# Performance work log

Hardware: AMD Instinct MI355X
Metric: run time of the kernel (lower is better)

Reference implementation:

```python
import jax, jax.numpy as jnp
import numpy as np

BN_EPS = 1e-5
SAMPLE_KEY = jax.random.key(42)


def setup_inputs() -> dict:
    key = jax.random.key(0)
    ks = jax.random.split(key, 12)
    B, W, E = 524288, 8, 4
    D = W * E  # 32, input dim of fc1

    def lin(k, fan_in, fan_out):
        k1, k2 = jax.random.split(k)
        bound = 1.0 / np.sqrt(fan_in)
        w = jax.random.uniform(k1, (fan_in, fan_out), jnp.float32, -bound, bound)
        b = jax.random.uniform(k2, (fan_out,), jnp.float32, -bound, bound)
        return w, b

    W1, b1 = lin(ks[0], D, 50)
    W2, b2 = lin(ks[1], 50, 30)
    W3, b3 = lin(ks[2], 30, 20)
    W4, b4 = lin(ks[3], 20, 15)
    W5, b5 = lin(ks[4], 15, W)
    # BatchNorm affine params (eval mode, running_mean=0, running_var=1)
    g1, be1 = jnp.ones((50,), jnp.float32), jnp.zeros((50,), jnp.float32)
    g2, be2 = jnp.ones((30,), jnp.float32), jnp.zeros((30,), jnp.float32)
    g3, be3 = jnp.ones((20,), jnp.float32), jnp.zeros((20,), jnp.float32)
    events = jax.random.normal(ks[5], (B, W, E), jnp.float32)
    return {"events": events,
            "W1": W1, "b1": b1, "g1": g1, "be1": be1,
            "W2": W2, "b2": b2, "g2": g2, "be2": be2,
            "W3": W3, "b3": b3, "g3": g3, "be3": be3,
            "W4": W4, "b4": b4, "W5": W5, "b5": b5}


def _bn_eval(x, g, b):
    # eval-mode BatchNorm1d with running_mean=0, running_var=1
    return x * (g / jnp.sqrt(1.0 + BN_EPS)) + b


def _probs(events, W1, b1, g1, be1, W2, b2, g2, be2, W3, b3, g3, be3, W4, b4, W5, b5):
    B = events.shape[0]
    x = events.reshape(B, -1)  # (B, window*event_size)
    h = jax.nn.relu(_bn_eval(x @ W1 + b1, g1, be1))
    h = jax.nn.relu(_bn_eval(h @ W2 + b2, g2, be2))
    h = jax.nn.relu(_bn_eval(h @ W3 + b3, g3, be3))
    h = jax.nn.relu(h @ W4 + b4)
    return jax.nn.sigmoid(h @ W5 + b5)  # (B, window_size)


def reference(events, W1, b1, g1, be1, W2, b2, g2, be2, W3, b3, g3, be3, W4, b4, W5, b5):
    p = _probs(events, W1, b1, g1, be1, W2, b2, g2, be2, W3, b3, g3, be3, W4, b4, W5, b5)
    # np.random.choice([0,1], p=[p, 1-p]) => P(choice=1) = 1 - p
    choice = jax.random.bernoulli(SAMPLE_KEY, 1.0 - p).astype(p.dtype)  # (B, W)
    chosen_events_np = 1.0 - choice
    flipped = jnp.abs(choice - p)            # prob of sampled outcome per element
    log_prob = jnp.log(jnp.prod(flipped, axis=1))  # (B,)
    return chosen_events_np, log_prob
```

## Files before the change

### kernel.cpp

```cpp
#include <hip/hip_runtime.h>
#include <math.h>

#define THREADS 256
#define TPW 4
#define ROWS_PER_BLOCK 256
#define P_MARGIN 2e-4f
#define FIXCAP 64

typedef float f32x4 __attribute__((ext_vector_type(4)));
typedef short short8 __attribute__((ext_vector_type(8)));
union Frag { unsigned u[4]; short8 s; };

#define FR1 0
#define FR2 2048
#define FR3 4096
#define FR4 5120
#define FR5 6144
#define VB1 6656
#define VS1 6708
#define VE1 6760
#define VB2 6812
#define VS2 6844
#define VE2 6876
#define VB3 6908
#define VS3 6928
#define VE3 6948
#define VB4 6968
#define VB5 6984
#define PZ  6992
#define WPOOL 7024

__device__ __forceinline__ void tf2x32(unsigned x0, unsigned x1,
                                       unsigned &o0, unsigned &o1) {
  const unsigned k0 = 0u;
  const unsigned k1 = 42u;
  const unsigned k2 = 0x1BD11BDAu ^ k0 ^ k1;
  x0 += k0; x1 += k1;
#define TF_R(r) { x0 += x1; x1 = (x1 << (r)) | (x1 >> (32 - (r))); x1 ^= x0; }
  TF_R(13) TF_R(15) TF_R(26) TF_R(6)
  x0 += k1; x1 += k2 + 1u;
  TF_R(17) TF_R(29) TF_R(16) TF_R(24)
  x0 += k2; x1 += k0 + 2u;
  TF_R(13) TF_R(15) TF_R(26) TF_R(6)
  x0 += k0; x1 += k1 + 3u;
  TF_R(17) TF_R(29) TF_R(16) TF_R(24)
  x0 += k1; x1 += k2 + 4u;
  TF_R(13) TF_R(15) TF_R(26) TF_R(6)
  x0 += k2; x1 += k0 + 5u;
#undef TF_R
  o0 = x0; o1 = x1;
}

__device__ __forceinline__ unsigned rtnb(float v) {
  unsigned b = __float_as_uint(v);
  return (b + 0x7FFFu + ((b >> 16) & 1u)) & 0xFFFF0000u;
}

__device__ __forceinline__ unsigned cvtpk(float a, float b) {
  unsigned r;
  asm("v_cvt_pk_bf16_f32 %0, %1, %2" : "=v"(r) : "v"(a), "v"(b));
  return r;
}

__device__ __forceinline__ void pack8(const float f[8], short8 &H, short8 &L) {
  Frag h, l;
#pragma unroll
  for (int d = 0; d < 4; ++d) {
    unsigned hd = cvtpk(f[2 * d], f[2 * d + 1]);
    h.u[d] = hd;
    float r0 = f[2 * d]     - __uint_as_float(hd << 16);
    float r1 = f[2 * d + 1] - __uint_as_float(hd & 0xFFFF0000u);
    l.u[d] = cvtpk(r0, r1);
  }
  H = h.s; L = l.s;
}

__device__ __forceinline__ f32x4 mfma16(short8 a, short8 b, f32x4 c) {
  return __builtin_amdgcn_mfma_f32_16x16x32_bf16(a, b, c, 0, 0, 0);
}

__device__ __forceinline__ short8 ldfrag(const float *sW, int dwoff) {
  return *reinterpret_cast<const short8 *>(sW + dwoff);
}
__device__ __forceinline__ f32x4 ldv4(const float *sW, int dwoff) {
  return *reinterpret_cast<const f32x4 *>(sW + dwoff);
}

template <int K, int N, int NT, int FB, bool PERM>
__device__ __forceinline__ void stageA(const float *__restrict__ W,
                                       float *sW, int t) {
  for (int i = t; i < K * N; i += THREADS) {
    int k = i / N, n = i - k * N;
    float v = W[i];
    unsigned hb = rtnb(v);
    unsigned lb = rtnb(v - __uint_as_float(hb));
    int kt = k >> 5, g = (k >> 3) & 3, e = k & 7, d = e >> 1, par = e & 1;
    int tile, r;
    if (PERM) {
      int pg = n >> 5, m = n & 31, tt = (m >> 2) & 1;
      r = ((m >> 3) << 2) | (m & 3);
      tile = pg * 2 + tt;
    } else {
      tile = n >> 4; r = n & 15;
    }
    int lane = g * 16 + r;
    int dwhi = FB + (kt * NT + tile) * 512 + lane * 4 + d;
    unsigned short *hp = reinterpret_cast<unsigned short *>(sW);
    hp[2 * dwhi + par] = (unsigned short)(hb >> 16);
    hp[2 * (dwhi + 256) + par] = (unsigned short)(lb >> 16);
  }
}

__device__ __forceinline__ void bnpack(f32x4 a0, f32x4 a1, const float *sW,
                                       int vs, int ve, int g,
                                       short8 &H, short8 &L) {
  f32x4 sc0 = ldv4(sW, vs + g * 8),     of0 = ldv4(sW, ve + g * 8);
  f32x4 sc1 = ldv4(sW, vs + g * 8 + 4), of1 = ldv4(sW, ve + g * 8 + 4);
  float f[8];
#pragma unroll
  for (int q = 0; q < 4; ++q) {
    f[q]     = fmaxf(fmaf(a0[q], sc0[q], of0[q]), 0.f);
    f[4 + q] = fmaxf(fmaf(a1[q], sc1[q], of1[q]), 0.f);
  }
  pack8(f, H, L);
}

__global__ __launch_bounds__(THREADS, 2)
void wtf_kernel(const float* __restrict__ events,
                const float* __restrict__ W1, const float* __restrict__ b1,
                const float* __restrict__ g1, const float* __restrict__ be1,
                const float* __restrict__ W2, const float* __restrict__ b2,
                const float* __restrict__ g2, const float* __restrict__ be2,
                const float* __restrict__ W3, const float* __restrict__ b3,
                const float* __restrict__ g3, const float* __restrict__ be3,
                const float* __restrict__ W4, const float* __restrict__ b4,
                const float* __restrict__ W5, const float* __restrict__ b5,
                float* __restrict__ out_chosen,
                float* __restrict__ out_logp,
                int B) {
  __shared__ float sW[WPOOL];
  __shared__ unsigned s_cnt;
  __shared__ unsigned s_rows[FIXCAP];
  __shared__ double sA[64];
  __shared__ double sB[64];
  __shared__ double sF[8];

  const int t = threadIdx.x;
  const float rden = (float)(1.0 / sqrt(1.0 + 1e-5));

  if (t == 0) s_cnt = 0;
  for (int i = t; i < WPOOL; i += THREADS) sW[i] = 0.f;
  __syncthreads();
  stageA<32, 50, 4, FR1, true>(W1, sW, t);
  stageA<50, 30, 2, FR2, true>(W2, sW, t);
  stageA<30, 20, 2, FR3, true>(W3, sW, t);
  stageA<20, 15, 2, FR4, true>(W4, sW, t);
  stageA<15,  8, 1, FR5, false>(W5, sW, t);
  if (t < 50)                  { sW[VB1 + t] = b1[t]; sW[VS1 + t] = g1[t] * rden; sW[VE1 + t] = be1[t]; }
  else if (t >= 64 && t < 94)  { int i = t - 64;  sW[VB2 + i] = b2[i]; sW[VS2 + i] = g2[i] * rden; sW[VE2 + i] = be2[i]; }
  else if (t >= 128 && t < 148){ int i = t - 128; sW[VB3 + i] = b3[i]; sW[VS3 + i] = g3[i] * rden; sW[VE3 + i] = be3[i]; }
  else if (t >= 192 && t < 207){ sW[VB4 + (t - 192)] = b4[t - 192]; }
  else if (t >= 224 && t < 232){ sW[VB5 + (t - 224)] = b5[t - 224]; }
  __syncthreads();

  const int w = t >> 6, lane = t & 63;
  const int c = lane & 15, g = lane >> 4;
  const int labase = lane * 4;

  const int wrow0 = blockIdx.x * ROWS_PER_BLOCK + w * (TPW * 16);
  const float4 *xp = reinterpret_cast<const float4 *>(
      events + (size_t)(wrow0 + c) * 32 + g * 8);

  f32x4 aa[TPW];

#pragma unroll
  for (int tt = 0; tt < TPW; ++tt) {
    float4 xa = xp[tt * 128], xb = xp[tt * 128 + 1];
    float xf[8] = {xa.x, xa.y, xa.z, xa.w, xb.x, xb.y, xb.z, xb.w};
    short8 Xh, Xl; pack8(xf, Xh, Xl);

    f32x4 a1[4];
#pragma unroll
    for (int ti = 0; ti < 4; ++ti) {
      f32x4 acc = ldv4(sW, VB1 + (ti >> 1) * 32 + g * 8 + (ti & 1) * 4);
      short8 wh = ldfrag(sW, FR1 + ti * 512 + labase);
      short8 wl = ldfrag(sW, FR1 + ti * 512 + 256 + labase);
      acc = mfma16(wh, Xl, acc);
      acc = mfma16(wl, Xh, acc);
      a1[ti] = mfma16(wh, Xh, acc);
    }

    short8 B2h[2], B2l[2];
    bnpack(a1[0], a1[1], sW, VS1,      VE1,      g, B2h[0], B2l[0]);
    bnpack(a1[2], a1[3], sW, VS1 + 32, VE1 + 32, g, B2h[1], B2l[1]);

    f32x4 a2[2];
#pragma unroll
    for (int ti = 0; ti < 2; ++ti) {
      f32x4 acc = ldv4(sW, VB2 + g * 8 + ti * 4);
#pragma unroll
      for (int kt = 0; kt < 2; ++kt) {
        short8 wh = ldfrag(sW, FR2 + (kt * 2 + ti) * 512 + labase);
        short8 wl = ldfrag(sW, FR2 + (kt * 2 + ti) * 512 + 256 + labase);
        acc = mfma16(wh, B2l[kt], acc);
        acc = mfma16(wl, B2h[kt], acc);
        acc = mfma16(wh, B2h[kt], acc);
      }
      a2[ti] = acc;
    }

    short8 B3h, B3l;
    bnpack(a2[0], a2[1], sW, VS2, VE2, g, B3h, B3l);

    f32x4 a3[2];
#pragma unroll
    for (int ti = 0; ti < 2; ++ti) {
      f32x4 acc = ldv4(sW, VB3 + g * 8 + ti * 4);
      short8 wh = ldfrag(sW, FR3 + ti * 512 + labase);
      short8 wl = ldfrag(sW, FR3 + ti * 512 + 256 + labase);
      acc = mfma16(wh, B3l, acc);
      acc = mfma16(wl, B3h, acc);
      a3[ti] = mfma16(wh, B3h, acc);
    }

    short8 B4h, B4l;
    bnpack(a3[0], a3[1], sW, VS3, VE3, g, B4h, B4l);

    f32x4 a4[2];
#pragma unroll
    for (int ti = 0; ti < 2; ++ti) {
      f32x4 acc = ldv4(sW, VB4 + g * 8 + ti * 4);
      short8 wh = ldfrag(sW, FR4 + ti * 512 + labase);
      short8 wl = ldfrag(sW, FR4 + ti * 512 + 256 + labase);
      acc = mfma16(wh, B4l, acc);
      acc = mfma16(wl, B4h, acc);
      a4[ti] = mfma16(wh, B4h, acc);
    }

    short8 B5h, B5l;
    {
      float f[8];
#pragma unroll
      for (int q = 0; q < 4; ++q) {
        f[q]     = fmaxf(a4[0][q], 0.f);
        f[4 + q] = fmaxf(a4[1][q], 0.f);
      }
      pack8(f, B5h, B5l);
    }

    {
      f32x4 acc = ldv4(sW, VB5 + g * 4);
      short8 wh = ldfrag(sW, FR5 + labase);
      short8 wl = ldfrag(sW, FR5 + 256 + labase);
      acc = mfma16(wh, B5l, acc);
      acc = mfma16(wl, B5h, acc);
      aa[tt] = mfma16(wh, B5h, acc);
    }
  }

#pragma unroll
  for (int tt = 0; tt < TPW; ++tt) {
    const int row = wrow0 + tt * 16 + c;
    float s2v = __shfl_xor(aa[tt][2], 32);
    float s3v = __shfl_xor(aa[tt][3], 32);
    float l0 = (g < 2) ? aa[tt][0] : s2v;
    float l1 = (g < 2) ? aa[tt][1] : s3v;
    const int base = ((g & 1) << 2) | ((g >> 1) << 1);
    float p0 = 1.f / (1.f + __expf(-l0));
    float p1 = 1.f / (1.f + __expf(-l1));
    unsigned o0, o1, q0, q1;
    tf2x32(0u, 8u * (unsigned)row + (unsigned)base,      o0, o1);
    tf2x32(0u, 8u * (unsigned)row + (unsigned)base + 1u, q0, q1);
    float u0 = __uint_as_float(0x3F800000u | ((o0 ^ o1) >> 9)) - 1.f;
    float u1 = __uint_as_float(0x3F800000u | ((q0 ^ q1) >> 9)) - 1.f;
    float th0 = 1.f - p0, th1 = 1.f - p1;
    bool c0 = u0 < th0, c1 = u1 < th1;
    bool need = (fabsf(u0 - th0) < P_MARGIN) || (fabsf(u1 - th1) < P_MARGIN);
    float prod = (c0 ? th0 : p0) * (c1 ? th1 : p1);
    prod *= __shfl_xor(prod, 16);
    prod *= __shfl_xor(prod, 32);
    float2 chv = make_float2(c0 ? 0.f : 1.f, c1 ? 0.f : 1.f);
    *reinterpret_cast<float2 *>(out_chosen + (size_t)row * 8 + base) = chv;
    if (g == 0) out_logp[row] = __logf(prod);
    if (need) {
      unsigned i = atomicAdd(&s_cnt, 1u);
      if (i < FIXCAP) s_rows[i] = (unsigned)row;
    }
  }

  __syncthreads();
  unsigned cnt = s_cnt;
  if (cnt > FIXCAP) cnt = FIXCAP;
  if (cnt == 0) return;

  const double denom = sqrt(1.0 + 1e-5);
  for (unsigned r = 0; r < cnt; ++r) {
    const int rb = (int)s_rows[r];

    if (t < 32) sA[t] = (double)events[(size_t)rb * 32 + t];
    __syncthreads();

    double v = 0.0;
    if (t < 50) {
#pragma unroll
      for (int k = 0; k < 32; ++k) v = fma(sA[k], (double)W1[k * 50 + t], v);
      v += (double)b1[t];
      v = v * ((double)g1[t] / denom) + (double)be1[t];
      v = v > 0.0 ? v : 0.0;
    }
    __syncthreads();
    if (t < 50) sB[t] = v;
    __syncthreads();

    v = 0.0;
    if (t < 30) {
#pragma unroll
      for (int k = 0; k < 50; ++k) v = fma(sB[k], (double)W2[k * 30 + t], v);
      v += (double)b2[t];
      v = v * ((double)g2[t] / denom) + (double)be2[t];
      v = v > 0.0 ? v : 0.0;
    }
    __syncthreads();
    if (t < 30) sA[t] = v;
    __syncthreads();

    v = 0.0;
    if (t < 20) {
#pragma unroll
      for (int k = 0; k < 30; ++k) v = fma(sA[k], (double)W3[k * 20 + t], v);
      v += (double)b3[t];
      v = v * ((double)g3[t] / denom) + (double)be3[t];
      v = v > 0.0 ? v : 0.0;
    }
    __syncthreads();
    if (t < 20) sB[t] = v;
    __syncthreads();

    v = 0.0;
    if (t < 15) {
#pragma unroll
      for (int k = 0; k < 20; ++k) v = fma(sB[k], (double)W4[k * 15 + t], v);
      v += (double)b4[t];
      v = v > 0.0 ? v : 0.0;
    }
    __syncthreads();
    if (t < 15) sA[t] = v;
    __syncthreads();

    if (t < 8) {
      v = 0.0;
#pragma unroll
      for (int k = 0; k < 15; ++k) v = fma(sA[k], (double)W5[k * 8 + t], v);
      v += (double)b5[t];
      double p = 1.0 / (1.0 + exp(-v));
      unsigned j = 8u * (unsigned)rb + (unsigned)t, o0, o1;
      tf2x32(0u, j, o0, o1);
      unsigned bits = o0 ^ o1;
      float u = __uint_as_float(0x3F800000u | (bits >> 9)) - 1.f;
      double thr = 1.0 - p;
      bool choice = ((double)u < thr);
      out_chosen[(size_t)rb * 8 + t] = choice ? 0.f : 1.f;
      sF[t] = choice ? thr : p;
    }
    __syncthreads();
    if (t == 0) {
      double prod = 1.0;
      for (int w2 = 0; w2 < 8; ++w2) prod *= sF[w2];
      out_logp[rb] = (float)log(prod);
    }
    __syncthreads();
  }
}

extern "C" void kernel_launch(void* const* d_in, const int* in_sizes, int n_in,
                              void* d_out, int out_size, void* d_ws, size_t ws_size,
                              hipStream_t stream) {
  const float* events = (const float*)d_in[0];
  const float* W1  = (const float*)d_in[1];
  const float* b1  = (const float*)d_in[2];
  const float* g1  = (const float*)d_in[3];
  const float* be1 = (const float*)d_in[4];
  const float* W2  = (const float*)d_in[5];
  const float* b2  = (const float*)d_in[6];
  const float* g2  = (const float*)d_in[7];
  const float* be2 = (const float*)d_in[8];
  const float* W3  = (const float*)d_in[9];
  const float* b3  = (const float*)d_in[10];
  const float* g3  = (const float*)d_in[11];
  const float* be3 = (const float*)d_in[12];
  const float* W4  = (const float*)d_in[13];
  const float* b4  = (const float*)d_in[14];
  const float* W5  = (const float*)d_in[15];
  const float* b5  = (const float*)d_in[16];

  const int B = in_sizes[0] / 32;
  float* out = (float*)d_out;
  float* out_chosen = out;
  float* out_logp   = out + (size_t)B * 8;

  const int blocks = (B + ROWS_PER_BLOCK - 1) / ROWS_PER_BLOCK;
  hipLaunchKernelGGL(wtf_kernel, dim3(blocks), dim3(THREADS), 0, stream,
                     events, W1, b1, g1, be1, W2, b2, g2, be2,
                     W3, b3, g3, be3, W4, b4, W5, b5,
                     out_chosen, out_logp, B);
}
```

Before: 216.1 us.

## Prebuild packed weight image once and hoist layer-4/5 fragments to registers

Adds a single-block pack kernel that converts all weights into the split-bf16 MFMA fragment layout in a workspace buffer. Each main-kernel block then copies that image into LDS with float4 loads, replacing the per-block zeroing, scatter and conversion. The small layer-4 and layer-5 weight fragments are also loaded once into registers instead of being reread from LDS on every tile. The cost is an extra kernel launch, a dependency on the workspace being large enough (with a fallback when it is not), and added register pressure.

```diff
diff --git a/kernel.cpp b/kernel.cpp
--- a/kernel.cpp
+++ b/kernel.cpp
@@ -86,9 +86,9 @@
   return *reinterpret_cast<const f32x4 *>(sW + dwoff);
 }
 
-template <int K, int N, int NT, int FB, bool PERM>
+template <int K, int N, int NT, int FB>
 __device__ __forceinline__ void stageA(const float *__restrict__ W,
-                                       float *sW, int t) {
+                                       unsigned short *hp, int t, bool perm) {
   for (int i = t; i < K * N; i += THREADS) {
     int k = i / N, n = i - k * N;
     float v = W[i];
@@ -96,7 +96,7 @@
     unsigned lb = rtnb(v - __uint_as_float(hb));
     int kt = k >> 5, g = (k >> 3) & 3, e = k & 7, d = e >> 1, par = e & 1;
     int tile, r;
-    if (PERM) {
+    if (perm) {
       int pg = n >> 5, m = n & 31, tt = (m >> 2) & 1;
       r = ((m >> 3) << 2) | (m & 3);
       tile = pg * 2 + tt;
@@ -105,24 +105,45 @@
     }
     int lane = g * 16 + r;
     int dwhi = FB + (kt * NT + tile) * 512 + lane * 4 + d;
-    unsigned short *hp = reinterpret_cast<unsigned short *>(sW);
     hp[2 * dwhi + par] = (unsigned short)(hb >> 16);
     hp[2 * (dwhi + 256) + par] = (unsigned short)(lb >> 16);
   }
 }
 
-__device__ __forceinline__ void bnpack(f32x4 a0, f32x4 a1, const float *sW,
-                                       int vs, int ve, int g,
-                                       short8 &H, short8 &L) {
-  f32x4 sc0 = ldv4(sW, vs + g * 8),     of0 = ldv4(sW, ve + g * 8);
-  f32x4 sc1 = ldv4(sW, vs + g * 8 + 4), of1 = ldv4(sW, ve + g * 8 + 4);
-  float f[8];
-#pragma unroll
-  for (int q = 0; q < 4; ++q) {
-    f[q]     = fmaxf(fmaf(a0[q], sc0[q], of0[q]), 0.f);
-    f[4 + q] = fmaxf(fmaf(a1[q], sc1[q], of1[q]), 0.f);
-  }
-  pack8(f, H, L);
+__device__ __forceinline__ void build_image(
+    float *img, int t,
+    const float *W1, const float *b1, const float *g1, const float *be1,
+    const float *W2, const float *b2, const float *g2, const float *be2,
+    const float *W3, const float *b3, const float *g3, const float *be3,
+    const float *W4, const float *b4, const float *W5, const float *b5) {
+  const float rden = (float)(1.0 / sqrt(1.0 + 1e-5));
+  for (int i = t; i < WPOOL; i += THREADS) img[i] = 0.f;
+  __syncthreads();
+  unsigned short *hp = reinterpret_cast<unsigned short *>(img);
+  stageA<32, 50, 4, FR1>(W1, hp, t, true);
+  stageA<50, 30, 2, FR2>(W2, hp, t, true);
+  stageA<30, 20, 2, FR3>(W3, hp, t, true);
+  stageA<20, 15, 2, FR4>(W4, hp, t, true);
+  stageA<15,  8, 1, FR5>(W5, hp, t, false);
+  if (t < 50)                  { img[VB1 + t] = b1[t]; img[VS1 + t] = g1[t] * rden; img[VE1 + t] = be1[t]; }
+  else if (t >= 64 && t < 94)  { int i = t - 64;  img[VB2 + i] = b2[i]; img[VS2 + i] = g2[i] * rden; img[VE2 + i] = be2[i]; }
+  else if (t >= 128 && t < 148){ int i = t - 128; img[VB3 + i] = b3[i]; img[VS3 + i] = g3[i] * rden; img[VE3 + i] = be3[i]; }
+  else if (t >= 192 && t < 207){ img[VB4 + (t - 192)] = b4[t - 192]; }
+  else if (t >= 224 && t < 232){ img[VB5 + (t - 224)] = b5[t - 224]; }
+}
+
+__global__ __launch_bounds__(THREADS, 1)
+void pack_kernel(const float* __restrict__ W1, const float* __restrict__ b1,
+                 const float* __restrict__ g1, const float* __restrict__ be1,
+                 const float* __restrict__ W2, const float* __restrict__ b2,
+                 const float* __restrict__ g2, const float* __restrict__ be2,
+                 const float* __restrict__ W3, const float* __restrict__ b3,
+                 const float* __restrict__ g3, const float* __restrict__ be3,
+                 const float* __restrict__ W4, const float* __restrict__ b4,
+                 const float* __restrict__ W5, const float* __restrict__ b5,
+                 float* __restrict__ img) {
+  build_image(img, threadIdx.x, W1, b1, g1, be1, W2, b2, g2, be2,
+              W3, b3, g3, be3, W4, b4, W5, b5);
 }
 
 __global__ __launch_bounds__(THREADS, 2)
@@ -135,6 +156,7 @@
                 const float* __restrict__ g3, const float* __restrict__ be3,
                 const float* __restrict__ W4, const float* __restrict__ b4,
                 const float* __restrict__ W5, const float* __restrict__ b5,
+                const float* __restrict__ img,
                 float* __restrict__ out_chosen,
                 float* __restrict__ out_logp,
                 int B) {
@@ -146,26 +168,28 @@
   __shared__ double sF[8];
 
   const int t = threadIdx.x;
-  const float rden = (float)(1.0 / sqrt(1.0 + 1e-5));
 
   if (t == 0) s_cnt = 0;
-  for (int i = t; i < WPOOL; i += THREADS) sW[i] = 0.f;
-  __syncthreads();
-  stageA<32, 50, 4, FR1, true>(W1, sW, t);
-  stageA<50, 30, 2, FR2, true>(W2, sW, t);
-  stageA<30, 20, 2, FR3, true>(W3, sW, t);
-  stageA<20, 15, 2, FR4, true>(W4, sW, t);
-  stageA<15,  8, 1, FR5, false>(W5, sW, t);
-  if (t < 50)                  { sW[VB1 + t] = b1[t]; sW[VS1 + t] = g1[t] * rden; sW[VE1 + t] = be1[t]; }
-  else if (t >= 64 && t < 94)  { int i = t - 64;  sW[VB2 + i] = b2[i]; sW[VS2 + i] = g2[i] * rden; sW[VE2 + i] = be2[i]; }
-  else if (t >= 128 && t < 148){ int i = t - 128; sW[VB3 + i] = b3[i]; sW[VS3 + i] = g3[i] * rden; sW[VE3 + i] = be3[i]; }
-  else if (t >= 192 && t < 207){ sW[VB4 + (t - 192)] = b4[t - 192]; }
-  else if (t >= 224 && t < 232){ sW[VB5 + (t - 224)] = b5[t - 224]; }
+  if (img) {
+    const float4 *s4 = reinterpret_cast<const float4 *>(img);
+    float4 *d4 = reinterpret_cast<float4 *>(sW);
+    for (int i = t; i < WPOOL / 4; i += THREADS) d4[i] = s4[i];
+  } else {
+    build_image(sW, t, W1, b1, g1, be1, W2, b2, g2, be2,
+                W3, b3, g3, be3, W4, b4, W5, b5);
+  }
   __syncthreads();
 
   const int w = t >> 6, lane = t & 63;
   const int c = lane & 15, g = lane >> 4;
   const int labase = lane * 4;
+
+  const short8 F4h0 = ldfrag(sW, FR4 + 0 * 512 + labase);
+  const short8 F4l0 = ldfrag(sW, FR4 + 0 * 512 + 256 + labase);
+  const short8 F4h1 = ldfrag(sW, FR4 + 1 * 512 + labase);
+  const short8 F4l1 = ldfrag(sW, FR4 + 1 * 512 + 256 + labase);
+  const short8 F5h  = ldfrag(sW, FR5 + labase);
+  const short8 F5l  = ldfrag(sW, FR5 + 256 + labase);
 
   const int wrow0 = blockIdx.x * ROWS_PER_BLOCK + w * (TPW * 16);
   const float4 *xp = reinterpret_cast<const float4 *>(
@@ -191,8 +215,25 @@
     }
 
     short8 B2h[2], B2l[2];
-    bnpack(a1[0], a1[1], sW, VS1,      VE1,      g, B2h[0], B2l[0]);
-    bnpack(a1[2], a1[3], sW, VS1 + 32, VE1 + 32, g, B2h[1], B2l[1]);
+    {
+      f32x4 sc0 = ldv4(sW, VS1 + g * 8),      of0 = ldv4(sW, VE1 + g * 8);
+      f32x4 sc1 = ldv4(sW, VS1 + g * 8 + 4),  of1 = ldv4(sW, VE1 + g * 8 + 4);
+      float f[8];
+#pragma unroll
+      for (int q = 0; q < 4; ++q) {
+        f[q]     = fmaxf(fmaf(a1[0][q], sc0[q], of0[q]), 0.f);
+        f[4 + q] = fmaxf(fmaf(a1[1][q], sc1[q], of1[q]), 0.f);
+      }
+      pack8(f, B2h[0], B2l[0]);
+      f32x4 sc2 = ldv4(sW, VS1 + 32 + g * 8),     of2 = ldv4(sW, VE1 + 32 + g * 8);
+      f32x4 sc3 = ldv4(sW, VS1 + 32 + g * 8 + 4), of3 = ldv4(sW, VE1 + 32 + g * 8 + 4);
+#pragma unroll
+      for (int q = 0; q < 4; ++q) {
+        f[q]     = fmaxf(fmaf(a1[2][q], sc2[q], of2[q]), 0.f);
+        f[4 + q] = fmaxf(fmaf(a1[3][q], sc3[q], of3[q]), 0.f);
+      }
+      pack8(f, B2h[1], B2l[1]);
+    }
 
     f32x4 a2[2];
 #pragma unroll
@@ -210,7 +251,17 @@
     }
 
     short8 B3h, B3l;
-    bnpack(a2[0], a2[1], sW, VS2, VE2, g, B3h, B3l);
+    {
+      f32x4 sc0 = ldv4(sW, VS2 + g * 8),     of0 = ldv4(sW, VE2 + g * 8);
+      f32x4 sc1 = ldv4(sW, VS2 + g * 8 + 4), of1 = ldv4(sW, VE2 + g * 8 + 4);
+      float f[8];
+#pragma unroll
+      for (int q = 0; q < 4; ++q) {
+        f[q]     = fmaxf(fmaf(a2[0][q], sc0[q], of0[q]), 0.f);
+        f[4 + q] = fmaxf(fmaf(a2[1][q], sc1[q], of1[q]), 0.f);
+      }
+      pack8(f, B3h, B3l);
+    }
 
     f32x4 a3[2];
 #pragma unroll
@@ -224,17 +275,28 @@
     }
 
     short8 B4h, B4l;
-    bnpack(a3[0], a3[1], sW, VS3, VE3, g, B4h, B4l);
+    {
+      f32x4 sc0 = ldv4(sW, VS3 + g * 8),     of0 = ldv4(sW, VE3 + g * 8);
+      f32x4 sc1 = ldv4(sW, VS3 + g * 8 + 4), of1 = ldv4(sW, VE3 + g * 8 + 4);
+      float f[8];
+#pragma unroll
+      for (int q = 0; q < 4; ++q) {
+        f[q]     = fmaxf(fmaf(a3[0][q], sc0[q], of0[q]), 0.f);
+        f[4 + q] = fmaxf(fmaf(a3[1][q], sc1[q], of1[q]), 0.f);
+      }
+      pack8(f, B4h, B4l);
+    }
 
     f32x4 a4[2];
-#pragma unroll
-    for (int ti = 0; ti < 2; ++ti) {
-      f32x4 acc = ldv4(sW, VB4 + g * 8 + ti * 4);
-      short8 wh = ldfrag(sW, FR4 + ti * 512 + labase);
-      short8 wl = ldfrag(sW, FR4 + ti * 512 + 256 + labase);
-      acc = mfma16(wh, B4l, acc);
-      acc = mfma16(wl, B4h, acc);
-      a4[ti] = mfma16(wh, B4h, acc);
+    {
+      f32x4 acc0 = ldv4(sW, VB4 + g * 8);
+      acc0 = mfma16(F4h0, B4l, acc0);
+      acc0 = mfma16(F4l0, B4h, acc0);
+      a4[0] = mfma16(F4h0, B4h, acc0);
+      f32x4 acc1 = ldv4(sW, VB4 + g * 8 + 4);
+      acc1 = mfma16(F4h1, B4l, acc1);
+      acc1 = mfma16(F4l1, B4h, acc1);
+      a4[1] = mfma16(F4h1, B4h, acc1);
     }
 
     short8 B5h, B5l;
@@ -250,11 +312,9 @@
 
     {
       f32x4 acc = ldv4(sW, VB5 + g * 4);
-      short8 wh = ldfrag(sW, FR5 + labase);
-      short8 wl = ldfrag(sW, FR5 + 256 + labase);
-      acc = mfma16(wh, B5l, acc);
-      acc = mfma16(wl, B5h, acc);
-      aa[tt] = mfma16(wh, B5h, acc);
+      acc = mfma16(F5h, B5l, acc);
+      acc = mfma16(F5l, B5h, acc);
+      aa[tt] = mfma16(F5h, B5h, acc);
     }
   }
 
@@ -398,9 +458,17 @@
   float* out_chosen = out;
   float* out_logp   = out + (size_t)B * 8;
 
+  float* img = (ws_size >= (size_t)WPOOL * sizeof(float)) ? (float*)d_ws
+                                                          : nullptr;
+  if (img) {
+    hipLaunchKernelGGL(pack_kernel, dim3(1), dim3(THREADS), 0, stream,
+                       W1, b1, g1, be1, W2, b2, g2, be2,
+                       W3, b3, g3, be3, W4, b4, W5, b5, img);
+  }
+
   const int blocks = (B + ROWS_PER_BLOCK - 1) / ROWS_PER_BLOCK;
   hipLaunchKernelGGL(wtf_kernel, dim3(blocks), dim3(THREADS), 0, stream,
                      events, W1, b1, g1, be1, W2, b2, g2, be2,
                      W3, b3, g3, be3, W4, b4, W5, b5,
-                     out_chosen, out_logp, B);
-}
+                     img, out_chosen, out_logp, B);
+}
```

New measurement: 222.8 us. 1.03x slower.
